# Kernel optimization log

Measured on AMD Instinct MI355X. Metric: run time of the kernel, lower is better.

## Reference

```python
import jax, jax.numpy as jnp
import numpy as np
import math

D_MODEL = 768
H = 12
D_FF = 3072
HEAD_DIM = D_MODEL // H
EPS = 1e-5


def setup_inputs() -> dict:
    key = jax.random.key(0)
    ks = jax.random.split(key, 12)
    s = 1.0 / math.sqrt(D_MODEL)
    inp = {
        "x": jax.random.normal(ks[0], (8, 1024, D_MODEL), dtype=jnp.float32),
        # attention projections (stored as [d_in, d_out])
        "wq": jax.random.normal(ks[1], (D_MODEL, D_MODEL), jnp.float32) * s,
        "bq": jnp.zeros((D_MODEL,), jnp.float32),
        "wk": jax.random.normal(ks[2], (D_MODEL, D_MODEL), jnp.float32) * s,
        "bk": jnp.zeros((D_MODEL,), jnp.float32),
        "wv": jax.random.normal(ks[3], (D_MODEL, D_MODEL), jnp.float32) * s,
        "bv": jnp.zeros((D_MODEL,), jnp.float32),
        "wo": jax.random.normal(ks[4], (D_MODEL, D_MODEL), jnp.float32) * s,
        "bo": jnp.zeros((D_MODEL,), jnp.float32),
        # FFN
        "w1": jax.random.normal(ks[5], (D_MODEL, D_FF), jnp.float32) * s,
        "b1": jnp.zeros((D_FF,), jnp.float32),
        "w2": jax.random.normal(ks[6], (D_FF, D_MODEL), jnp.float32) * (1.0 / math.sqrt(D_FF)),
        "b2": jnp.zeros((D_MODEL,), jnp.float32),
        # LayerNormalization scalar params (gemma/beta) for the two residual norms
        "g1": jnp.ones((1,), jnp.float32),
        "be1": jnp.zeros((1,), jnp.float32),
        "g2": jnp.ones((1,), jnp.float32),
        "be2": jnp.zeros((1,), jnp.float32),
    }
    return inp


def _layernorm(x, g, b):
    # torch: mean and UNBIASED std over last dim; divide by (std + eps)
    mean = jnp.mean(x, axis=-1, keepdims=True)
    std = jnp.std(x, axis=-1, keepdims=True, ddof=1)
    return g * (x - mean) / (std + EPS) + b


def _attention(x, wq, bq, wk, bk, wv, bv, wo, bo):
    B, N, _ = x.shape
    q = (x @ wq + bq).reshape(B, N, H, HEAD_DIM)
    k = (x @ wk + bk).reshape(B, N, H, HEAD_DIM)
    v = (x @ wv + bv).reshape(B, N, H, HEAD_DIM)
    scores = jnp.einsum("bqhd,bkhd->bhqk", q, k) / math.sqrt(HEAD_DIM)
    w = jax.nn.softmax(scores, axis=-1)
    out = jnp.einsum("bhqk,bkhd->bqhd", w, v).reshape(B, N, D_MODEL)
    return out @ wo + bo


def _ffn(x, w1, b1, w2, b2):
    return (jax.nn.gelu(x @ w1 + b1, approximate=False)) @ w2 + b2


def reference(x, wq, bq, wk, bk, wv, bv, wo, bo, w1, b1, w2, b2, g1, be1, g2, be2):
    # pre-LN residual block 1: attention
    x = x + _attention(_layernorm(x, g1, be1), wq, bq, wk, bk, wv, bv, wo, bo)
    # pre-LN residual block 2: FFN
    x = x + _ffn(_layernorm(x, g2, be2), w1, b1, w2, b2)
    return x
```

## Files before the change

### kernel.cpp

```cpp
#include <hip/hip_runtime.h>
#include <hip/hip_bf16.h>
#include <math.h>

typedef unsigned short u16;
typedef unsigned int u32;
typedef u16 u16x8 __attribute__((ext_vector_type(8)));
typedef __bf16 bf16x8 __attribute__((ext_vector_type(8)));
typedef float f32x4 __attribute__((ext_vector_type(4)));

#define MODE_GELU 1
#define MODE_RESF32 2
#define MODE_QKV 3

template <typename T, typename F>
__device__ __forceinline__ T bitcast(F f) { return __builtin_bit_cast(T, f); }

__device__ __forceinline__ u16 f2bf(float f) {
    unsigned int u = __float_as_uint(f);
    u = (u + 0x7fffu + ((u >> 16) & 1u)) >> 16;
    return (u16)u;
}

__device__ __forceinline__ u32 packbf(float lo, float hi) {
    return (u32)f2bf(lo) | ((u32)f2bf(hi) << 16);
}

__device__ __forceinline__ float fast_gelu(float x) {
    const float arg = x * (2.30220775f + 0.10294329f * x * x);
    const float e = exp2f(arg);
    return x * (1.0f - __builtin_amdgcn_rcpf(e + 1.0f));
}

__device__ __forceinline__ void gl_lds16(const u16* g, u16* l) {
    __builtin_amdgcn_global_load_lds(
        (const __attribute__((address_space(1))) unsigned int*)(const void*)g,
        (__attribute__((address_space(3))) unsigned int*)(void*)l,
        16, 0, 0);
}

__device__ __forceinline__ void stage64(const u16* __restrict__ src, int stride,
                                        u16* __restrict__ lds, int t)
{
    const int wave = t >> 6, lane = t & 63;
#pragma unroll
    for (int i = 0; i < 2; i++) {
        const int row = i * 32 + wave * 8 + (lane >> 3);
        const int s = lane & 7;
        const int f = (((row >> 3) & 1) << 2) | (row & 3);
        gl_lds16(src + (size_t)row * stride + (size_t)((s ^ f) << 3),
                 lds + i * 2048 + wave * 512);
    }
}

__global__ __launch_bounds__(256) void prep_kernel(
    const float* __restrict__ wq, const float* __restrict__ wk,
    const float* __restrict__ wv, const float* __restrict__ wo,
    const float* __restrict__ w1, const float* __restrict__ w2,
    const float* __restrict__ bq, const float* __restrict__ bk,
    const float* __restrict__ bv,
    u16* __restrict__ wqkvT, u16* __restrict__ woT,
    u16* __restrict__ w1T, u16* __restrict__ w2T, float* __restrict__ bqkv,
    const float* __restrict__ X, u16* __restrict__ Y,
    const float* __restrict__ gp, const float* __restrict__ bp)
{
    const int blk = blockIdx.x;
    if (blk >= 6921) {
        __shared__ float sbuf[8];
        const int row = blk - 6921, t = threadIdx.x;
        const float* xr = X + (size_t)row * 768;
        float v0 = xr[t], v1 = xr[t + 256], v2 = xr[t + 512];
        float s = v0 + v1 + v2;
        float q = v0 * v0 + v1 * v1 + v2 * v2;
#pragma unroll
        for (int m = 1; m < 64; m <<= 1) {
            s += __shfl_xor(s, m, 64);
            q += __shfl_xor(q, m, 64);
        }
        const int wave = t >> 6, lane = t & 63;
        if (lane == 0) { sbuf[wave] = s; sbuf[4 + wave] = q; }
        __syncthreads();
        s = sbuf[0] + sbuf[1] + sbuf[2] + sbuf[3];
        q = sbuf[4] + sbuf[5] + sbuf[6] + sbuf[7];
        const float mean = s * (1.0f / 768.0f);
        float ssd = fmaxf(q - 768.0f * mean * mean, 0.0f);
        const float stdv = sqrtf(ssd * (1.0f / 767.0f));
        const float scale = gp[0] / (stdv + 1e-5f);
        const float beta = bp[0];
        u16* yr = Y + (size_t)row * 768;
        yr[t]       = f2bf((v0 - mean) * scale + beta);
        yr[t + 256] = f2bf((v1 - mean) * scale + beta);
        yr[t + 512] = f2bf((v2 - mean) * scale + beta);
        return;
    }
    if (blk >= 6912) {
        const int t = (blk - 6912) * 256 + threadIdx.x;
        if (t < 2304)
            bqkv[t] = t < 768 ? bq[t] : (t < 1536 ? bk[t - 768] : bv[t - 1536]);
        return;
    }
    const float* W; u16* WT; int Krows, Ncols, lt;
    if (blk < 576)       { W = wq; WT = wqkvT;                       Krows = 768;  Ncols = 768;  lt = blk; }
    else if (blk < 1152) { W = wk; WT = wqkvT + (size_t)768 * 768;   Krows = 768;  Ncols = 768;  lt = blk - 576; }
    else if (blk < 1728) { W = wv; WT = wqkvT + (size_t)1536 * 768;  Krows = 768;  Ncols = 768;  lt = blk - 1152; }
    else if (blk < 2304) { W = wo; WT = woT;                         Krows = 768;  Ncols = 768;  lt = blk - 1728; }
    else if (blk < 4608) { W = w1; WT = w1T;                         Krows = 768;  Ncols = 3072; lt = blk - 2304; }
    else                 { W = w2; WT = w2T;                         Krows = 3072; Ncols = 768;  lt = blk - 4608; }
    const int ktiles = Krows >> 5;
    const int k0 = (lt % ktiles) * 32, n0 = (lt / ktiles) * 32;

    __shared__ float tile[32][33];
    const int tx = threadIdx.x & 31, ty = threadIdx.x >> 5;
#pragma unroll
    for (int j = 0; j < 32; j += 8)
        tile[ty + j][tx] = W[(size_t)(k0 + ty + j) * Ncols + n0 + tx];
    __syncthreads();
#pragma unroll
    for (int j = 0; j < 32; j += 8)
        WT[(size_t)(n0 + ty + j) * Krows + k0 + tx] = f2bf(tile[tx][ty + j]);
}

__global__ __launch_bounds__(256) void ln_kernel(
    const float* __restrict__ X, u16* __restrict__ Y,
    const float* __restrict__ gp, const float* __restrict__ bp)
{
    __shared__ float sbuf[8];
    const int row = blockIdx.x, t = threadIdx.x;
    const float* xr = X + (size_t)row * 768;
    float v0 = xr[t], v1 = xr[t + 256], v2 = xr[t + 512];
    float s = v0 + v1 + v2;
    float q = v0 * v0 + v1 * v1 + v2 * v2;
#pragma unroll
    for (int m = 1; m < 64; m <<= 1) {
        s += __shfl_xor(s, m, 64);
        q += __shfl_xor(q, m, 64);
    }
    const int wave = t >> 6, lane = t & 63;
    if (lane == 0) { sbuf[wave] = s; sbuf[4 + wave] = q; }
    __syncthreads();
    s = sbuf[0] + sbuf[1] + sbuf[2] + sbuf[3];
    q = sbuf[4] + sbuf[5] + sbuf[6] + sbuf[7];
    const float mean = s * (1.0f / 768.0f);
    float ssd = fmaxf(q - 768.0f * mean * mean, 0.0f);
    const float stdv = sqrtf(ssd * (1.0f / 767.0f));
    const float scale = gp[0] / (stdv + 1e-5f);
    const float beta = bp[0];
    u16* yr = Y + (size_t)row * 768;
    yr[t]       = f2bf((v0 - mean) * scale + beta);
    yr[t + 256] = f2bf((v1 - mean) * scale + beta);
    yr[t + 512] = f2bf((v2 - mean) * scale + beta);
}

template <int MODE>
__global__ __launch_bounds__(256) void gemm_kernel(
    const u16* __restrict__ A, const u16* __restrict__ BT,
    const float* __restrict__ bias, const float* __restrict__ res,
    void* __restrict__ out0, void* __restrict__ out1, void* __restrict__ out2,
    int M, int N, int K)
{
    __shared__ u16 sh[2][2][128 * 64];
    u16* shp = &sh[0][0][0];
    const int t = threadIdx.x;
    const int lane = t & 63, wave = t >> 6;
    const int wr = wave >> 1, wc = wave & 1;
    const int g = lane >> 4, c = lane & 15;

    const int lin = blockIdx.x + blockIdx.y * gridDim.x;
    const int xcd = lin & 7, idx = lin >> 3;
    const int bm = xcd * 8 + (idx & 7);
    const int bn = idx >> 3;

    const int srow = wave * 32 + (lane >> 3);
    const u16* Ag = A + (size_t)(bm * 128 + srow) * K;
    const u16* Bg = BT + (size_t)(bn * 128 + srow) * K;

    const int fc = (((c >> 3) & 1) << 2) | (c & 3);
    const int xs0 = (g ^ fc) << 3;
    const int xs1 = ((4 + g) ^ fc) << 3;

    f32x4 acc[4][4] = {};
    const int nk = K >> 6;

    const int sl = lane & 7;
    int sco[4];
#pragma unroll
    for (int it = 0; it < 4; it++)
        sco[it] = ((sl ^ (((it & 1) << 2) | ((lane >> 3) & 3))) << 3);

#define STAGE_AB(buf, k0)                                                     \
    {                                                                         \
        _Pragma("unroll")                                                     \
        for (int it = 0; it < 4; it++) {                                      \
            gl_lds16(Ag + (size_t)(it * 8) * K + (k0) + sco[it], &sh[buf][0][wave * 2048 + it * 512]); \
            gl_lds16(Bg + (size_t)(it * 8) * K + (k0) + sco[it], &sh[buf][1][wave * 2048 + it * 512]); \
        }                                                                     \
    }

    STAGE_AB(0, 0);
    __syncthreads();

    for (int ks = 0; ks < nk; ks++) {
        const int cur = ks & 1;
        if (ks + 1 < nk) STAGE_AB(cur ^ 1, (ks + 1) << 6);
        const u16* Asb = sh[cur][0];
        const u16* Bsb = sh[cur][1];
        __builtin_amdgcn_s_setprio(1);
#pragma unroll
        for (int kk = 0; kk < 2; kk++) {
            const int xo = kk ? xs1 : xs0;
            bf16x8 af[4], bfr[4];
#pragma unroll
            for (int m = 0; m < 4; m++)
                af[m] = *(const bf16x8*)&Asb[(wr * 64 + m * 16 + c) * 64 + xo];
#pragma unroll
            for (int n = 0; n < 4; n++)
                bfr[n] = *(const bf16x8*)&Bsb[(wc * 64 + n * 16 + c) * 64 + xo];
#pragma unroll
            for (int m = 0; m < 4; m++)
#pragma unroll
                for (int n = 0; n < 4; n++)
                    acc[m][n] = __builtin_amdgcn_mfma_f32_16x16x32_bf16(
                        af[m], bfr[n], acc[m][n], 0, 0, 0);
        }
        __builtin_amdgcn_s_setprio(0);
        __syncthreads();
    }
#undef STAGE_AB

    if constexpr (MODE == MODE_QKV) {
        if (bn >= 12) {
#pragma unroll
            for (int m = 0; m < 4; m++) {
#pragma unroll
                for (int n = 0; n < 4; n++) {
                    const int colL = wc * 64 + n * 16 + c;
                    const int rowLb = wr * 64 + m * 16 + 4 * g;
                    const float bv = bias[bn * 128 + colL];
                    const u32 x0 = packbf(acc[m][n][0] + bv, acc[m][n][1] + bv);
                    const u32 x1 = packbf(acc[m][n][2] + bv, acc[m][n][3] + bv);
                    const int elem = colL * 128 + (rowLb ^ ((colL & 15) << 3));
                    ((u32*)shp)[elem >> 1] = x0;
                    ((u32*)shp)[(elem >> 1) + 1] = x1;
                }
            }
            __syncthreads();
            const int bn_off = bn - 12;
            const int bb = bm >> 3, kvb = (bm & 7) * 128;
            const int j8 = (t & 7) * 8;
#pragma unroll
            for (int it = 0; it < 4; it++) {
                const int colL2 = it * 32 + (t >> 3);
                const int gcol = bn_off * 128 + colL2;
                const int hh = gcol >> 6, d = gcol & 63;
                const size_t obase = ((size_t)(bb * 12 + hh) << 16) + ((size_t)d << 10) + kvb;
                const int X = (colL2 & 15) << 3;
#pragma unroll
                for (int half = 0; half < 2; half++) {
                    const int rowL2 = half * 64 + j8;
                    const int elem = colL2 * 128 + (rowL2 ^ X);
                    *(u16x8*)((u16*)out2 + obase + rowL2) = *(const u16x8*)&shp[elem];
                }
            }
            return;
        }
    }

#pragma unroll
    for (int m = 0; m < 4; m++) {
        const int row = bm * 128 + wr * 64 + m * 16 + 4 * g;
#pragma unroll
        for (int n = 0; n < 4; n++) {
            const int col = bn * 128 + wc * 64 + n * 16 + c;
            const float bv = bias[col];
#pragma unroll
            for (int i = 0; i < 4; i++) {
                float v = acc[m][n][i] + bv;
                if constexpr (MODE == MODE_GELU) {
                    ((u16*)out0)[(size_t)(row + i) * N + col] = f2bf(fast_gelu(v));
                } else if constexpr (MODE == MODE_RESF32) {
                    const size_t idx = (size_t)(row + i) * N + col;
                    ((float*)out0)[idx] = v + res[idx];
                } else {
                    const int sect = (col >= 768) ? 1 : 0;
                    const int colm = col - sect * 768;
                    u16* dst = sect ? (u16*)out1 : (u16*)out0;
                    dst[(size_t)(row + i) * 768 + colm] = f2bf(v);
                }
            }
        }
    }
}

__global__ __launch_bounds__(256) void attn_kernel(
    const u16* __restrict__ Qg, const u16* __restrict__ Kg,
    const u16* __restrict__ Vt_g, u16* __restrict__ O)
{
    __shared__ u16 Kl[2][4096];
    __shared__ u16 Vl[2][4096];
    const int t = threadIdx.x, lane = t & 63, wave = t >> 6;
    const int g = lane >> 4, c = lane & 15;
    const int l = blockIdx.x;
    const int pos = l >> 3;
    const int b = l & 7, h = pos >> 4;
    const int qt = pos & 15;
    const int bh = b * 12 + h;
    const size_t rowb = (size_t)b * 1024;
    const int q0 = qt * 64 + wave * 16;

    bf16x8 qa[2];
    {
        const u16* qp = Qg + (rowb + q0 + c) * 768 + h * 64 + g * 8;
        u16x8 a0 = *(const u16x8*)qp;
        u16x8 a1 = *(const u16x8*)(qp + 32);
        bf16x8 va0, va1;
#pragma unroll
        for (int j = 0; j < 8; j++) {
            const float SC = 0.18033688011112042f;
            va0[j] = (__bf16)(__uint_as_float(((u32)a0[j]) << 16) * SC);
            va1[j] = (__bf16)(__uint_as_float(((u32)a1[j]) << 16) * SC);
        }
        qa[0] = va0; qa[1] = va1;
    }

    bf16x8 vone;
#pragma unroll
    for (int j = 0; j < 8; j++) vone[j] = (__bf16)1.0f;

    int kro[4], kxo[4], vro[4];
#pragma unroll
    for (int n = 0; n < 4; n++) {
        const int pr = ((n >> 1) << 5) + ((c >> 2) << 3) + ((n & 1) << 2) + (c & 3);
        kro[n] = pr << 6;
        kxo[n] = (((pr >> 3) & 1) << 2) | (pr & 3);
        vro[n] = (n * 16 + c) << 6;
    }
    const int vxo = (((c >> 3) & 1) << 2) | (c & 3);

    const u16* ksrc = Kg + rowb * 768 + h * 64;
    const u16* vsrc = Vt_g + (size_t)bh * 65536;

    float negm = 0.0f;
    f32x4 oa[4] = {};
    f32x4 lsum = {};
    const int srcb = (lane & 48) | ((lane >> 2) & 12);

    stage64(ksrc, 768, Kl[0], t);
    stage64(vsrc, 1024, Vl[0], t);
    __syncthreads();

    for (int kvt = 0; kvt < 16; ++kvt) {
        const u16* Kc = Kl[kvt & 1];
        const u16* Vc = Vl[kvt & 1];
        if (kvt < 15) {
            stage64(ksrc + (size_t)(kvt + 1) * 64 * 768, 768, Kl[(kvt + 1) & 1], t);
            stage64(vsrc + (kvt + 1) * 64, 1024, Vl[(kvt + 1) & 1], t);
        }

        f32x4 s0[4];
#pragma unroll
        for (int n = 0; n < 4; n++) {
            s0[n][0] = negm; s0[n][1] = negm; s0[n][2] = negm; s0[n][3] = negm;
        }
        __builtin_amdgcn_s_setprio(1);
#pragma unroll
        for (int n = 0; n < 4; n++) {
#pragma unroll
            for (int kk = 0; kk < 2; kk++) {
                const bf16x8 kf = *(const bf16x8*)&Kc[kro[n] + ((((kk << 2) + g) ^ kxo[n]) << 3)];
                s0[n] = __builtin_amdgcn_mfma_f32_16x16x32_bf16(kf, qa[kk], s0[n], 0, 0, 0);
            }
        }
        __builtin_amdgcn_s_setprio(0);

        bf16x8 pa00, pa01;
        {
            float mx = fmaxf(fmaxf(s0[0][0], s0[0][1]), s0[0][2]);
            mx = fmaxf(fmaxf(mx, s0[0][3]), s0[1][0]);
            mx = fmaxf(fmaxf(mx, s0[1][1]), s0[1][2]);
            mx = fmaxf(fmaxf(mx, s0[1][3]), s0[2][0]);
            mx = fmaxf(fmaxf(mx, s0[2][1]), s0[2][2]);
            mx = fmaxf(fmaxf(mx, s0[2][3]), s0[3][0]);
            mx = fmaxf(fmaxf(mx, s0[3][1]), s0[3][2]);
            mx = fmaxf(mx, s0[3][3]);
            mx = fmaxf(mx, __shfl_xor(mx, 16, 64));
            mx = fmaxf(mx, __shfl_xor(mx, 32, 64));
            if (!__all(mx <= 8.0f)) {
                const float delta = fmaxf(mx, 0.0f);
                const float rsc = exp2f(-delta);
                negm -= delta;
                f32x4 rq;
#pragma unroll
                for (int i = 0; i < 4; i++) rq[i] = __shfl(rsc, srcb + i, 64);
#pragma unroll
                for (int n = 0; n < 4; n++) oa[n] *= rq;
                lsum *= rq;
#pragma unroll
                for (int n = 0; n < 4; n++)
#pragma unroll
                    for (int i = 0; i < 4; i++) s0[n][i] -= delta;
            }
#pragma unroll
            for (int n = 0; n < 4; n++)
#pragma unroll
                for (int i = 0; i < 4; i++)
                    s0[n][i] = exp2f(s0[n][i]);
#pragma unroll
            for (int i = 0; i < 4; i++) {
                pa00[i] = (__bf16)s0[0][i]; pa00[4 + i] = (__bf16)s0[1][i];
                pa01[i] = (__bf16)s0[2][i]; pa01[4 + i] = (__bf16)s0[3][i];
            }
        }

        __builtin_amdgcn_s_setprio(1);
        lsum = __builtin_amdgcn_mfma_f32_16x16x32_bf16(pa00, vone, lsum, 0, 0, 0);
        lsum = __builtin_amdgcn_mfma_f32_16x16x32_bf16(pa01, vone, lsum, 0, 0, 0);
#pragma unroll
        for (int n = 0; n < 4; n++) {
#pragma unroll
            for (int kk = 0; kk < 2; kk++) {
                const bf16x8 vf = *(const bf16x8*)&Vc[vro[n] + ((((kk << 2) + g) ^ vxo) << 3)];
                oa[n] = __builtin_amdgcn_mfma_f32_16x16x32_bf16(kk ? pa01 : pa00, vf, oa[n], 0, 0, 0);
            }
        }
        __builtin_amdgcn_s_setprio(0);
        __syncthreads();
    }

#pragma unroll
    for (int i = 0; i < 4; i++) {
        const float ia_ = 1.0f / fmaxf(lsum[i], 1e-30f);
        const size_t ra_ = rowb + q0 + 4 * g + i;
#pragma unroll
        for (int n = 0; n < 4; n++)
            O[ra_ * 768 + h * 64 + n * 16 + c] = f2bf(oa[n][i] * ia_);
    }
}

extern "C" void kernel_launch(void* const* d_in, const int* in_sizes, int n_in,
                              void* d_out, int out_size, void* d_ws, size_t ws_size,
                              hipStream_t stream)
{
    const float* x   = (const float*)d_in[0];
    const float* wq  = (const float*)d_in[1];
    const float* bq  = (const float*)d_in[2];
    const float* wk  = (const float*)d_in[3];
    const float* bk  = (const float*)d_in[4];
    const float* wv  = (const float*)d_in[5];
    const float* bv  = (const float*)d_in[6];
    const float* wo  = (const float*)d_in[7];
    const float* bo  = (const float*)d_in[8];
    const float* w1  = (const float*)d_in[9];
    const float* b1  = (const float*)d_in[10];
    const float* w2  = (const float*)d_in[11];
    const float* b2  = (const float*)d_in[12];
    const float* g1  = (const float*)d_in[13];
    const float* be1 = (const float*)d_in[14];
    const float* g2  = (const float*)d_in[15];
    const float* be2 = (const float*)d_in[16];

    char* ws = (char*)d_ws;
    constexpr size_t O_WQKV = 0;
    constexpr size_t O_WO   = 3538944;
    constexpr size_t O_W1   = 4718592;
    constexpr size_t O_W2   = 9437184;
    constexpr size_t O_BQKV = 14155776;
    constexpr size_t O_XLN  = 14168064;
    constexpr size_t O_Q    = O_XLN + 12582912;
    constexpr size_t O_K    = O_Q + 12582912;
    constexpr size_t O_VT   = O_K + 12582912;
    constexpr size_t O_ATTN = O_VT + 12582912;
    constexpr size_t O_H    = O_ATTN + 12582912;
    constexpr size_t O_F    = O_XLN;
    constexpr size_t O_HLN  = O_ATTN;

    u16* wqkvT = (u16*)(ws + O_WQKV);
    u16* woT   = (u16*)(ws + O_WO);
    u16* w1T   = (u16*)(ws + O_W1);
    u16* w2T   = (u16*)(ws + O_W2);
    float* bqkv = (float*)(ws + O_BQKV);
    u16* xln   = (u16*)(ws + O_XLN);
    u16* Qb    = (u16*)(ws + O_Q);
    u16* Kb    = (u16*)(ws + O_K);
    u16* VTg   = (u16*)(ws + O_VT);
    u16* attnb = (u16*)(ws + O_ATTN);
    float* h   = (float*)(ws + O_H);
    u16* fb    = (u16*)(ws + O_F);
    u16* hln   = (u16*)(ws + O_HLN);

    dim3 blk(256);
    prep_kernel<<<6921 + 8192, blk, 0, stream>>>(wq, wk, wv, wo, w1, w2, bq, bk, bv,
                                                 wqkvT, woT, w1T, w2T, bqkv,
                                                 x, xln, g1, be1);
    gemm_kernel<MODE_QKV><<<dim3(64, 18), blk, 0, stream>>>(
        xln, wqkvT, bqkv, nullptr, Qb, Kb, VTg, 8192, 2304, 768);
    attn_kernel<<<1536, blk, 0, stream>>>(Qb, Kb, VTg, attnb);
    gemm_kernel<MODE_RESF32><<<dim3(64, 6), blk, 0, stream>>>(
        attnb, woT, bo, x, h, nullptr, nullptr, 8192, 768, 768);
    ln_kernel<<<8192, blk, 0, stream>>>(h, hln, g2, be2);
    gemm_kernel<MODE_GELU><<<dim3(64, 24), blk, 0, stream>>>(
        hln, w1T, b1, nullptr, fb, nullptr, nullptr, 8192, 3072, 768);
    gemm_kernel<MODE_RESF32><<<dim3(64, 6), blk, 0, stream>>>(
        fb, w2T, b2, h, (float*)d_out, nullptr, nullptr, 8192, 768, 3072);
}
```

Before: 238.5 us.

## Add dedicated 128x256 tile GEMM with 512 threads for FFN up-projection

Replaces the generic 128x128-tile GEMM for the FFN first layer (with GELU epilogue) with a specialized kernel. The new kernel uses 512 threads (8 waves), 128x256 output tiles, K-steps of 32, and a 4-deep LDS ring with loads issued two steps ahead. It also remaps block indices so that neighbouring M tiles share an XCD. The intent is more reuse per loaded tile, deeper prefetch, and better L2 locality, at the cost of more LDS per block (96KB) and fewer resident blocks.

```diff
diff --git a/kernel.cpp b/kernel.cpp
--- a/kernel.cpp
+++ b/kernel.cpp
@@ -285,6 +285,88 @@
                     u16* dst = sect ? (u16*)out1 : (u16*)out0;
                     dst[(size_t)(row + i) * 768 + colm] = f2bf(v);
                 }
+            }
+        }
+    }
+}
+
+__global__ __launch_bounds__(512) void gemm_k32_gelu(
+    const u16* __restrict__ A, const u16* __restrict__ BT,
+    const float* __restrict__ bias, u16* __restrict__ out0,
+    int M, int N, int K)
+{
+    __shared__ u16 sh[4][12288];
+    const int t = threadIdx.x;
+    const int lane = t & 63, wave = t >> 6;
+    const int wm = wave >> 2, wn = wave & 3;
+    const int g = lane >> 4, c = lane & 15;
+
+    const int lin = blockIdx.x + blockIdx.y * gridDim.x;
+    const int xcd = lin & 7, idx = lin >> 3;
+    const int bm = xcd * 8 + (idx & 7);
+    const int bn = idx >> 3;
+
+    const int srow = 16 * wave + (lane >> 2);
+    const int sxor = ((lane & 3) ^ ((lane >> 3) & 3)) << 3;
+    const u16* Ag = A + (size_t)(bm * 128 + srow) * K + sxor;
+    const u16* Bg = BT + (size_t)(bn * 256 + srow) * K + sxor;
+    const size_t BgS = (size_t)128 * K;
+
+    const int xo = ((g ^ ((c >> 1) & 3)) << 3);
+
+    f32x4 acc[4][4] = {};
+    const int nk = K >> 5;
+
+#define STG(buf, ks)                                                           \
+    {                                                                          \
+        gl_lds16(Ag + (size_t)(ks) * 32, &sh[buf][wave * 512]);                \
+        gl_lds16(Bg + (size_t)(ks) * 32, &sh[buf][4096 + wave * 512]);         \
+        gl_lds16(Bg + BgS + (size_t)(ks) * 32, &sh[buf][8192 + wave * 512]);   \
+    }
+
+    STG(0, 0);
+    STG(1, 1);
+
+    for (int ks = 0; ks < nk; ks++) {
+        if (ks + 2 < nk) {
+            STG((ks + 2) & 3, ks + 2);
+            asm volatile("s_waitcnt vmcnt(6)" ::: "memory");
+        } else if (ks + 1 < nk) {
+            asm volatile("s_waitcnt vmcnt(3)" ::: "memory");
+        } else {
+            asm volatile("s_waitcnt vmcnt(0)" ::: "memory");
+        }
+        __builtin_amdgcn_s_barrier();
+        const u16* buf = sh[ks & 3];
+        bf16x8 af[4], bfr[4];
+#pragma unroll
+        for (int m = 0; m < 4; m++)
+            af[m] = *(const bf16x8*)&buf[(wm * 64 + m * 16 + c) * 32 + xo];
+#pragma unroll
+        for (int n = 0; n < 4; n++)
+            bfr[n] = *(const bf16x8*)&buf[4096 + (wn * 64 + n * 16 + c) * 32 + xo];
+        __builtin_amdgcn_s_setprio(1);
+#pragma unroll
+        for (int m = 0; m < 4; m++)
+#pragma unroll
+            for (int n = 0; n < 4; n++)
+                acc[m][n] = __builtin_amdgcn_mfma_f32_16x16x32_bf16(
+                    af[m], bfr[n], acc[m][n], 0, 0, 0);
+        __builtin_amdgcn_s_setprio(0);
+    }
+#undef STG
+
+#pragma unroll
+    for (int m = 0; m < 4; m++) {
+        const int row = bm * 128 + wm * 64 + m * 16 + 4 * g;
+#pragma unroll
+        for (int n = 0; n < 4; n++) {
+            const int col = bn * 256 + wn * 64 + n * 16 + c;
+            const float bv = bias[col];
+#pragma unroll
+            for (int i = 0; i < 4; i++) {
+                float v = acc[m][n][i] + bv;
+                out0[(size_t)(row + i) * N + col] = f2bf(fast_gelu(v));
             }
         }
     }
@@ -496,8 +578,8 @@
     gemm_kernel<MODE_RESF32><<<dim3(64, 6), blk, 0, stream>>>(
         attnb, woT, bo, x, h, nullptr, nullptr, 8192, 768, 768);
     ln_kernel<<<8192, blk, 0, stream>>>(h, hln, g2, be2);
-    gemm_kernel<MODE_GELU><<<dim3(64, 24), blk, 0, stream>>>(
-        hln, w1T, b1, nullptr, fb, nullptr, nullptr, 8192, 3072, 768);
+    gemm_k32_gelu<<<dim3(64, 12), dim3(512), 0, stream>>>(
+        hln, w1T, b1, fb, 8192, 3072, 768);
     gemm_kernel<MODE_RESF32><<<dim3(64, 6), blk, 0, stream>>>(
         fb, w2T, b2, h, (float*)d_out, nullptr, nullptr, 8192, 768, 3072);
 }
```

Result: no change. 240.9 us (+1.0%).
